# Kernel tuning notes

Hardware: AMD Instinct MI355X
Metric: run time of the kernel (lower is better)

## Reference

```python
import jax, jax.numpy as jnp
import numpy as np

N_NODES = 50000


def _gcn_layer(x, W, b, src, dst, n_nodes):
    # x: [N, Fin] -> h: [N, Fout]
    h = x @ W
    # symmetric normalization deg^{-1/2} A_hat deg^{-1/2} (self-loops already in src/dst)
    deg = jax.ops.segment_sum(jnp.ones(src.shape[0], h.dtype), dst, num_segments=n_nodes)
    dis = jnp.where(deg > 0, jax.lax.rsqrt(deg), jnp.zeros_like(deg))
    norm = dis[src] * dis[dst]  # [E]
    msg = h[src] * norm[:, None]  # [E, Fout]
    out = jax.ops.segment_sum(msg, dst, num_segments=n_nodes)
    return out + b


def setup_inputs() -> dict:
    key = jax.random.key(0)
    k1, k2, k3, k4 = jax.random.split(key, 4)
    in_ch, hid, out_ch = 128, 128, 64
    x = jax.random.normal(k1, (N_NODES, in_ch), dtype=jnp.float32)
    edge_index = jax.random.randint(k2, (2, 800000), 0, N_NODES, dtype=jnp.int64)
    # glorot-style init for the linear weights
    W1 = jax.random.normal(k3, (in_ch, hid), dtype=jnp.float32) * (1.0 / np.sqrt(in_ch))
    b1 = jnp.zeros((hid,), dtype=jnp.float32)
    W2 = jax.random.normal(k4, (hid, out_ch), dtype=jnp.float32) * (1.0 / np.sqrt(hid))
    b2 = jnp.zeros((out_ch,), dtype=jnp.float32)
    return {"x": x, "edge_index": edge_index, "W1": W1, "b1": b1, "W2": W2, "b2": b2}


def reference(x, edge_index, W1, b1, W2, b2):
    n = x.shape[0]
    loops = jnp.arange(n, dtype=edge_index.dtype)
    src = jnp.concatenate([edge_index[0], loops])
    dst = jnp.concatenate([edge_index[1], loops])
    h = jnp.tanh(_gcn_layer(x, W1, b1, src, dst, n))
    return _gcn_layer(h, W2, b2, src, dst, n)
```

## Files before the change

### kernel.cpp

```cpp
#include <hip/hip_runtime.h>
#include <math.h>


__global__ void detect_kernel(const int* __restrict__ ei32, int* __restrict__ flag) {
    if (blockIdx.x == 0 && threadIdx.x == 0) {
        int is64 = 1;
        for (int k = 1; k < 64; k += 2)
            if (ei32[k] != 0) { is64 = 0; break; }
        *flag = is64;
    }
}

__global__ __launch_bounds__(256) void normalize_kernel(const int* __restrict__ ei32,
                                                        const int* __restrict__ flag,
                                                        int* __restrict__ out, int n2,
                                                        int* __restrict__ hist, int nh) {
    const int is64 = *flag;
    for (int i = blockIdx.x * blockDim.x + threadIdx.x; i < n2;
         i += gridDim.x * blockDim.x) {
        out[i] = is64 ? ei32[2 * i] : ei32[i];
        if (i < nh) hist[i] = 0;
    }
}

__global__ __launch_bounds__(256) void hist_kernel(const int* __restrict__ dst, int E,
                                                   int* __restrict__ hist) {
    for (int i = blockIdx.x * blockDim.x + threadIdx.x; i < E;
         i += gridDim.x * blockDim.x) {
        atomicAdd(&hist[dst[i]], 1);
    }
}

__global__ __launch_bounds__(256) void scan1_kernel(const int* __restrict__ hist,
                                                    int* __restrict__ row_start,
                                                    int* __restrict__ partial, int n) {
    __shared__ int tmp[256];
    int t = threadIdx.x;
    int i = blockIdx.x * 256 + t;
    int v = (i < n) ? hist[i] : 0;
    tmp[t] = v;
    __syncthreads();
    for (int off = 1; off < 256; off <<= 1) {
        int add = (t >= off) ? tmp[t - off] : 0;
        __syncthreads();
        tmp[t] += add;
        __syncthreads();
    }
    if (i < n) row_start[i] = tmp[t] - v;
    if (t == 255) partial[blockIdx.x] = tmp[255];
}

__global__ __launch_bounds__(256) void scan2_kernel(const int* __restrict__ partial,
                                                    int* __restrict__ offsets, int nb) {
    __shared__ int tmp[256];
    int t = threadIdx.x;
    int v = (t < nb) ? partial[t] : 0;
    tmp[t] = v;
    __syncthreads();
    for (int off = 1; off < 256; off <<= 1) {
        int add = (t >= off) ? tmp[t - off] : 0;
        __syncthreads();
        tmp[t] += add;
        __syncthreads();
    }
    if (t < nb) offsets[t] = tmp[t] - v;
}

__global__ __launch_bounds__(256) void scan3_kernel(int* __restrict__ row_start,
                                                    const int* __restrict__ offsets,
                                                    const int* __restrict__ hist,
                                                    float* __restrict__ dis,
                                                    int* __restrict__ cursor,
                                                    int n, int E) {
    int i = blockIdx.x * 256 + threadIdx.x;
    if (i < n) {
        row_start[i] += offsets[i >> 8];
        dis[i] = rsqrtf((float)(hist[i] + 1));
        cursor[i] = 0;
    }
    if (i == 0) row_start[n] = E;
}

__global__ __launch_bounds__(256) void scatter_kernel(const int* __restrict__ src,
                                                      const int* __restrict__ dst, int E,
                                                      const int* __restrict__ row_start,
                                                      int* __restrict__ cursor,
                                                      int* __restrict__ csr_src) {
    for (int i = blockIdx.x * blockDim.x + threadIdx.x; i < E;
         i += gridDim.x * blockDim.x) {
        int d = dst[i];
        int pos = atomicAdd(&cursor[d], 1);
        csr_src[row_start[d] + pos] = src[i];
    }
}

template <int BM, int BN, int TM, int TN>
__global__ __launch_bounds__(256) void gemm_tile(const float* __restrict__ A,
                                                 const float* __restrict__ B,
                                                 const float* __restrict__ scale,
                                                 float* __restrict__ C,
                                                 int M, int K, int N) {
    constexpr int BK = 32;
    constexpr int TX = BN / TN;
    constexpr int TY = BM / TM;
    static_assert(TX * TY == 256, "256 threads");
    const int t = threadIdx.x;
    const int tx = t % TX;
    const int ty = t / TX;
    const int row0 = blockIdx.x * BM;

    __shared__ float As[BK][BM + 4];
    __shared__ float Bs[BK][BN + 4];

    float acc[TM][TN];
#pragma unroll
    for (int i = 0; i < TM; i++)
#pragma unroll
        for (int j = 0; j < TN; j++) acc[i][j] = 0.f;

    for (int k0 = 0; k0 < K; k0 += BK) {
        constexpr int A4 = BM * BK / 4;
#pragma unroll
        for (int idx4 = t; idx4 < A4; idx4 += 256) {
            int r = idx4 / (BK / 4);
            int c4 = idx4 % (BK / 4);
            float4 v = make_float4(0.f, 0.f, 0.f, 0.f);
            int gr = row0 + r;
            if (gr < M) v = *(const float4*)&A[(size_t)gr * K + k0 + c4 * 4];
            As[c4 * 4 + 0][r] = v.x;
            As[c4 * 4 + 1][r] = v.y;
            As[c4 * 4 + 2][r] = v.z;
            As[c4 * 4 + 3][r] = v.w;
        }
        constexpr int B4 = BK * BN / 4;
#pragma unroll
        for (int idx4 = t; idx4 < B4; idx4 += 256) {
            int r = idx4 / (BN / 4);
            int c4 = idx4 % (BN / 4);
            float4 v = *(const float4*)&B[(size_t)(k0 + r) * N + c4 * 4];
            *(float4*)&Bs[r][c4 * 4] = v;
        }
        __syncthreads();

#pragma unroll 4
        for (int kk = 0; kk < BK; kk++) {
            float a[TM], b[TN];
#pragma unroll
            for (int i = 0; i < TM; i += 4)
                *(float4*)&a[i] = *(const float4*)&As[kk][ty * TM + i];
#pragma unroll
            for (int j = 0; j < TN; j += 4)
                *(float4*)&b[j] = *(const float4*)&Bs[kk][tx * TN + j];
#pragma unroll
            for (int i = 0; i < TM; i++)
#pragma unroll
                for (int j = 0; j < TN; j++) acc[i][j] += a[i] * b[j];
        }
        __syncthreads();
    }

#pragma unroll
    for (int i = 0; i < TM; i++) {
        int gr = row0 + ty * TM + i;
        if (gr < M) {
            float sc = scale[gr];
#pragma unroll
            for (int j = 0; j < TN; j += 4) {
                float4 v = make_float4(acc[i][j] * sc, acc[i][j + 1] * sc,
                                       acc[i][j + 2] * sc, acc[i][j + 3] * sc);
                *(float4*)&C[(size_t)gr * N + tx * TN + j] = v;
            }
        }
    }
}

__global__ __launch_bounds__(256) void agg1_kernel(const float* __restrict__ hs,
                                                   const float* __restrict__ dis,
                                                   const int* __restrict__ row_start,
                                                   const int* __restrict__ csr_src,
                                                   const float* __restrict__ b1,
                                                   float* __restrict__ hout, int n) {
    int wid = threadIdx.x >> 6;
    int lane = threadIdx.x & 63;
    int node = blockIdx.x * 4 + wid;
    if (node >= n) return;

    const float2* hv = (const float2*)hs;
    float2 acc = hv[(size_t)node * 64 + lane];

    int e0 = row_start[node], e1 = row_start[node + 1];
    int e = e0;
    for (; e + 4 <= e1; e += 4) {
        int s0 = csr_src[e + 0];
        int s1 = csr_src[e + 1];
        int s2 = csr_src[e + 2];
        int s3 = csr_src[e + 3];
        float2 v0 = hv[(size_t)s0 * 64 + lane];
        float2 v1 = hv[(size_t)s1 * 64 + lane];
        float2 v2 = hv[(size_t)s2 * 64 + lane];
        float2 v3 = hv[(size_t)s3 * 64 + lane];
        acc.x += (v0.x + v1.x) + (v2.x + v3.x);
        acc.y += (v0.y + v1.y) + (v2.y + v3.y);
    }
    for (; e < e1; ++e) {
        int s = csr_src[e];
        float2 v = hv[(size_t)s * 64 + lane];
        acc.x += v.x;
        acc.y += v.y;
    }
    float dd = dis[node];
    float2 bb = ((const float2*)b1)[lane];
    float2 o;
    o.x = tanhf(acc.x * dd + bb.x);
    o.y = tanhf(acc.y * dd + bb.y);
    ((float2*)hout)[(size_t)node * 64 + lane] = o;
}

__global__ __launch_bounds__(256) void agg2_kernel(const float* __restrict__ hs,
                                                   const float* __restrict__ dis,
                                                   const int* __restrict__ row_start,
                                                   const int* __restrict__ csr_src,
                                                   const float* __restrict__ b2,
                                                   float* __restrict__ out, int n) {
    int wid = threadIdx.x >> 6;
    int lane = threadIdx.x & 63;
    int node = blockIdx.x * 4 + wid;
    if (node >= n) return;

    float acc = hs[(size_t)node * 64 + lane];

    int e0 = row_start[node], e1 = row_start[node + 1];
    int e = e0;
    for (; e + 4 <= e1; e += 4) {
        int s0 = csr_src[e + 0];
        int s1 = csr_src[e + 1];
        int s2 = csr_src[e + 2];
        int s3 = csr_src[e + 3];
        float v0 = hs[(size_t)s0 * 64 + lane];
        float v1 = hs[(size_t)s1 * 64 + lane];
        float v2 = hs[(size_t)s2 * 64 + lane];
        float v3 = hs[(size_t)s3 * 64 + lane];
        acc += (v0 + v1) + (v2 + v3);
    }
    for (; e < e1; ++e) {
        acc += hs[(size_t)csr_src[e] * 64 + lane];
    }
    out[(size_t)node * 64 + lane] = acc * dis[node] + b2[lane];
}

extern "C" void kernel_launch(void* const* d_in, const int* in_sizes, int n_in,
                              void* d_out, int out_size, void* d_ws, size_t ws_size,
                              hipStream_t stream) {
    const float* x  = (const float*)d_in[0];
    const int*   ei = (const int*)d_in[1];
    const float* W1 = (const float*)d_in[2];
    const float* b1 = (const float*)d_in[3];
    const float* W2 = (const float*)d_in[4];
    const float* b2 = (const float*)d_in[5];

    const int hid    = in_sizes[3];
    const int in_ch  = in_sizes[2] / hid;
    const int out_ch = in_sizes[5];
    const int N      = in_sizes[0] / in_ch;
    const int E      = in_sizes[1] / 2;

    char* wsp = (char*)d_ws;
    auto alloc = [&](size_t bytes) -> char* {
        char* p = wsp;
        wsp += (bytes + 255) & ~(size_t)255;
        return p;
    };
    float* h1        = (float*)alloc((size_t)N * hid * 4);
    float* hmid      = (float*)alloc((size_t)N * hid * 4);
    float* h2        = (float*)alloc((size_t)N * out_ch * 4);
    int*   hist      = (int*)alloc((size_t)N * 4);
    int*   cursor    = (int*)alloc((size_t)N * 4);
    int*   row_start = (int*)alloc((size_t)(N + 1) * 4);
    float* dis       = (float*)alloc((size_t)N * 4);
    int*   partial   = (int*)alloc(1024);
    int*   offsets   = (int*)alloc(1024);
    int*   flag      = (int*)alloc(256);
    int*   enorm     = (int*)alloc((size_t)2 * E * 4);
    int*   csr_src   = (int*)alloc((size_t)E * 4);

    const int NB = (N + 255) / 256;

    detect_kernel<<<1, 64, 0, stream>>>(ei, flag);
    normalize_kernel<<<2048, 256, 0, stream>>>(ei, flag, enorm, 2 * E, hist, N);
    const int* esrc = enorm;
    const int* edst = enorm + E;

    hist_kernel<<<1024, 256, 0, stream>>>(edst, E, hist);
    scan1_kernel<<<NB, 256, 0, stream>>>(hist, row_start, partial, N);
    scan2_kernel<<<1, 256, 0, stream>>>(partial, offsets, NB);
    scan3_kernel<<<NB, 256, 0, stream>>>(row_start, offsets, hist, dis, cursor, N, E);
    scatter_kernel<<<1024, 256, 0, stream>>>(esrc, edst, E, row_start, cursor, csr_src);

    gemm_tile<128, 128, 8, 8><<<(N + 127) / 128, 256, 0, stream>>>(x, W1, dis, h1, N, in_ch, hid);
    agg1_kernel<<<(N + 3) / 4, 256, 0, stream>>>(h1, dis, row_start, csr_src, b1, hmid, N);

    gemm_tile<128, 64, 8, 4><<<(N + 127) / 128, 256, 0, stream>>>(hmid, W2, dis, h2, N, hid, out_ch);
    agg2_kernel<<<(N + 3) / 4, 256, 0, stream>>>(h2, dis, row_start, csr_src, b2,
                                                 (float*)d_out, N);
}
```

Baseline: 321.3 us.

## Store GEMM outputs in fp16 to halve gather traffic in aggregation

The two GEMMs now write their scaled node features as fp16 instead of fp32, and both aggregation kernels gather fp16 rows and accumulate in fp32. This halves the bytes moved by the random-access neighbour gathers, which dominate the aggregation cost. Edge-format detection is folded into the normalize kernel, removing one launch, and the aggregation kernels switch to a fixed 1280-block grid-stride loop. The cost is reduced precision in the intermediate features, which may push results past the tolerance.

```diff
diff --git a/kernel.cpp b/kernel.cpp
--- a/kernel.cpp
+++ b/kernel.cpp
@@ -1,21 +1,20 @@
 #include <hip/hip_runtime.h>
+#include <hip/hip_fp16.h>
 #include <math.h>
 
 
-__global__ void detect_kernel(const int* __restrict__ ei32, int* __restrict__ flag) {
-    if (blockIdx.x == 0 && threadIdx.x == 0) {
+__global__ __launch_bounds__(256) void normalize_kernel(const int* __restrict__ ei32,
+                                                        int* __restrict__ out, int n2,
+                                                        int* __restrict__ hist, int nh) {
+    __shared__ int s_is64;
+    if (threadIdx.x == 0) {
         int is64 = 1;
         for (int k = 1; k < 64; k += 2)
             if (ei32[k] != 0) { is64 = 0; break; }
-        *flag = is64;
-    }
-}
-
-__global__ __launch_bounds__(256) void normalize_kernel(const int* __restrict__ ei32,
-                                                        const int* __restrict__ flag,
-                                                        int* __restrict__ out, int n2,
-                                                        int* __restrict__ hist, int nh) {
-    const int is64 = *flag;
+        s_is64 = is64;
+    }
+    __syncthreads();
+    const int is64 = s_is64;
     for (int i = blockIdx.x * blockDim.x + threadIdx.x; i < n2;
          i += gridDim.x * blockDim.x) {
         out[i] = is64 ? ei32[2 * i] : ei32[i];
@@ -94,11 +93,11 @@
     }
 }
 
-template <int BM, int BN, int TM, int TN>
+template <int BM, int BN, int TM, int TN, bool HALF_OUT>
 __global__ __launch_bounds__(256) void gemm_tile(const float* __restrict__ A,
                                                  const float* __restrict__ B,
                                                  const float* __restrict__ scale,
-                                                 float* __restrict__ C,
+                                                 void* __restrict__ Cv,
                                                  int M, int K, int N) {
     constexpr int BK = 32;
     constexpr int TX = BN / TN;
@@ -164,88 +163,101 @@
         int gr = row0 + ty * TM + i;
         if (gr < M) {
             float sc = scale[gr];
-#pragma unroll
-            for (int j = 0; j < TN; j += 4) {
-                float4 v = make_float4(acc[i][j] * sc, acc[i][j + 1] * sc,
-                                       acc[i][j + 2] * sc, acc[i][j + 3] * sc);
-                *(float4*)&C[(size_t)gr * N + tx * TN + j] = v;
+            if constexpr (HALF_OUT) {
+                __half* C = (__half*)Cv;
+                __half2 tmp[TN / 2];
+#pragma unroll
+                for (int j = 0; j < TN; j += 2)
+                    tmp[j / 2] = __floats2half2_rn(acc[i][j] * sc, acc[i][j + 1] * sc);
+                if constexpr (TN == 8) {
+                    *(float4*)&C[(size_t)gr * N + tx * TN] = *(float4*)tmp;
+                } else {
+                    *(float2*)&C[(size_t)gr * N + tx * TN] = *(float2*)tmp;
+                }
+            } else {
+                float* C = (float*)Cv;
+#pragma unroll
+                for (int j = 0; j < TN; j += 4) {
+                    float4 v = make_float4(acc[i][j] * sc, acc[i][j + 1] * sc,
+                                           acc[i][j + 2] * sc, acc[i][j + 3] * sc);
+                    *(float4*)&C[(size_t)gr * N + tx * TN + j] = v;
+                }
             }
         }
     }
 }
 
-__global__ __launch_bounds__(256) void agg1_kernel(const float* __restrict__ hs,
+__global__ __launch_bounds__(256) void agg1_kernel(const __half* __restrict__ hs,
                                                    const float* __restrict__ dis,
                                                    const int* __restrict__ row_start,
                                                    const int* __restrict__ csr_src,
                                                    const float* __restrict__ b1,
                                                    float* __restrict__ hout, int n) {
-    int wid = threadIdx.x >> 6;
-    int lane = threadIdx.x & 63;
-    int node = blockIdx.x * 4 + wid;
-    if (node >= n) return;
-
-    const float2* hv = (const float2*)hs;
-    float2 acc = hv[(size_t)node * 64 + lane];
-
-    int e0 = row_start[node], e1 = row_start[node + 1];
-    int e = e0;
-    for (; e + 4 <= e1; e += 4) {
-        int s0 = csr_src[e + 0];
-        int s1 = csr_src[e + 1];
-        int s2 = csr_src[e + 2];
-        int s3 = csr_src[e + 3];
-        float2 v0 = hv[(size_t)s0 * 64 + lane];
-        float2 v1 = hv[(size_t)s1 * 64 + lane];
-        float2 v2 = hv[(size_t)s2 * 64 + lane];
-        float2 v3 = hv[(size_t)s3 * 64 + lane];
-        acc.x += (v0.x + v1.x) + (v2.x + v3.x);
-        acc.y += (v0.y + v1.y) + (v2.y + v3.y);
-    }
-    for (; e < e1; ++e) {
-        int s = csr_src[e];
-        float2 v = hv[(size_t)s * 64 + lane];
-        acc.x += v.x;
-        acc.y += v.y;
-    }
-    float dd = dis[node];
-    float2 bb = ((const float2*)b1)[lane];
-    float2 o;
-    o.x = tanhf(acc.x * dd + bb.x);
-    o.y = tanhf(acc.y * dd + bb.y);
-    ((float2*)hout)[(size_t)node * 64 + lane] = o;
-}
-
-__global__ __launch_bounds__(256) void agg2_kernel(const float* __restrict__ hs,
+    const int wid = threadIdx.x >> 6;
+    const int lane = threadIdx.x & 63;
+    const __half2* hv = (const __half2*)hs;
+
+    for (int node = blockIdx.x * 4 + wid; node < n; node += gridDim.x * 4) {
+        float2 acc = __half22float2(hv[(size_t)node * 64 + lane]);
+
+        int e0 = row_start[node], e1 = row_start[node + 1];
+        int e = e0;
+        for (; e + 4 <= e1; e += 4) {
+            int s0 = csr_src[e + 0];
+            int s1 = csr_src[e + 1];
+            int s2 = csr_src[e + 2];
+            int s3 = csr_src[e + 3];
+            float2 v0 = __half22float2(hv[(size_t)s0 * 64 + lane]);
+            float2 v1 = __half22float2(hv[(size_t)s1 * 64 + lane]);
+            float2 v2 = __half22float2(hv[(size_t)s2 * 64 + lane]);
+            float2 v3 = __half22float2(hv[(size_t)s3 * 64 + lane]);
+            acc.x += (v0.x + v1.x) + (v2.x + v3.x);
+            acc.y += (v0.y + v1.y) + (v2.y + v3.y);
+        }
+        for (; e < e1; ++e) {
+            float2 v = __half22float2(hv[(size_t)csr_src[e] * 64 + lane]);
+            acc.x += v.x;
+            acc.y += v.y;
+        }
+        float dd = dis[node];
+        float2 bb = ((const float2*)b1)[lane];
+        float2 o;
+        o.x = tanhf(acc.x * dd + bb.x);
+        o.y = tanhf(acc.y * dd + bb.y);
+        ((float2*)hout)[(size_t)node * 64 + lane] = o;
+    }
+}
+
+__global__ __launch_bounds__(256) void agg2_kernel(const __half* __restrict__ hs,
                                                    const float* __restrict__ dis,
                                                    const int* __restrict__ row_start,
                                                    const int* __restrict__ csr_src,
                                                    const float* __restrict__ b2,
                                                    float* __restrict__ out, int n) {
-    int wid = threadIdx.x >> 6;
-    int lane = threadIdx.x & 63;
-    int node = blockIdx.x * 4 + wid;
-    if (node >= n) return;
-
-    float acc = hs[(size_t)node * 64 + lane];
-
-    int e0 = row_start[node], e1 = row_start[node + 1];
-    int e = e0;
-    for (; e + 4 <= e1; e += 4) {
-        int s0 = csr_src[e + 0];
-        int s1 = csr_src[e + 1];
-        int s2 = csr_src[e + 2];
-        int s3 = csr_src[e + 3];
-        float v0 = hs[(size_t)s0 * 64 + lane];
-        float v1 = hs[(size_t)s1 * 64 + lane];
-        float v2 = hs[(size_t)s2 * 64 + lane];
-        float v3 = hs[(size_t)s3 * 64 + lane];
-        acc += (v0 + v1) + (v2 + v3);
-    }
-    for (; e < e1; ++e) {
-        acc += hs[(size_t)csr_src[e] * 64 + lane];
-    }
-    out[(size_t)node * 64 + lane] = acc * dis[node] + b2[lane];
+    const int wid = threadIdx.x >> 6;
+    const int lane = threadIdx.x & 63;
+
+    for (int node = blockIdx.x * 4 + wid; node < n; node += gridDim.x * 4) {
+        float acc = __half2float(hs[(size_t)node * 64 + lane]);
+
+        int e0 = row_start[node], e1 = row_start[node + 1];
+        int e = e0;
+        for (; e + 4 <= e1; e += 4) {
+            int s0 = csr_src[e + 0];
+            int s1 = csr_src[e + 1];
+            int s2 = csr_src[e + 2];
+            int s3 = csr_src[e + 3];
+            float v0 = __half2float(hs[(size_t)s0 * 64 + lane]);
+            float v1 = __half2float(hs[(size_t)s1 * 64 + lane]);
+            float v2 = __half2float(hs[(size_t)s2 * 64 + lane]);
+            float v3 = __half2float(hs[(size_t)s3 * 64 + lane]);
+            acc += (v0 + v1) + (v2 + v3);
+        }
+        for (; e < e1; ++e) {
+            acc += __half2float(hs[(size_t)csr_src[e] * 64 + lane]);
+        }
+        out[(size_t)node * 64 + lane] = acc * dis[node] + b2[lane];
+    }
 }
 
 extern "C" void kernel_launch(void* const* d_in, const int* in_sizes, int n_in,
@@ -270,23 +282,21 @@
         wsp += (bytes + 255) & ~(size_t)255;
         return p;
     };
-    float* h1        = (float*)alloc((size_t)N * hid * 4);
-    float* hmid      = (float*)alloc((size_t)N * hid * 4);
-    float* h2        = (float*)alloc((size_t)N * out_ch * 4);
+    __half* h1       = (__half*)alloc((size_t)N * hid * 2);
+    float*  hmid     = (float*)alloc((size_t)N * hid * 4);
+    __half* h2       = (__half*)alloc((size_t)N * out_ch * 2);
     int*   hist      = (int*)alloc((size_t)N * 4);
     int*   cursor    = (int*)alloc((size_t)N * 4);
     int*   row_start = (int*)alloc((size_t)(N + 1) * 4);
     float* dis       = (float*)alloc((size_t)N * 4);
     int*   partial   = (int*)alloc(1024);
     int*   offsets   = (int*)alloc(1024);
-    int*   flag      = (int*)alloc(256);
     int*   enorm     = (int*)alloc((size_t)2 * E * 4);
     int*   csr_src   = (int*)alloc((size_t)E * 4);
 
     const int NB = (N + 255) / 256;
 
-    detect_kernel<<<1, 64, 0, stream>>>(ei, flag);
-    normalize_kernel<<<2048, 256, 0, stream>>>(ei, flag, enorm, 2 * E, hist, N);
+    normalize_kernel<<<2048, 256, 0, stream>>>(ei, enorm, 2 * E, hist, N);
     const int* esrc = enorm;
     const int* edst = enorm + E;
 
@@ -296,10 +306,12 @@
     scan3_kernel<<<NB, 256, 0, stream>>>(row_start, offsets, hist, dis, cursor, N, E);
     scatter_kernel<<<1024, 256, 0, stream>>>(esrc, edst, E, row_start, cursor, csr_src);
 
-    gemm_tile<128, 128, 8, 8><<<(N + 127) / 128, 256, 0, stream>>>(x, W1, dis, h1, N, in_ch, hid);
-    agg1_kernel<<<(N + 3) / 4, 256, 0, stream>>>(h1, dis, row_start, csr_src, b1, hmid, N);
-
-    gemm_tile<128, 64, 8, 4><<<(N + 127) / 128, 256, 0, stream>>>(hmid, W2, dis, h2, N, hid, out_ch);
-    agg2_kernel<<<(N + 3) / 4, 256, 0, stream>>>(h2, dis, row_start, csr_src, b2,
-                                                 (float*)d_out, N);
-}
+    gemm_tile<128, 128, 8, 8, true><<<(N + 127) / 128, 256, 0, stream>>>(
+        x, W1, dis, h1, N, in_ch, hid);
+    agg1_kernel<<<1280, 256, 0, stream>>>(h1, dis, row_start, csr_src, b1, hmid, N);
+
+    gemm_tile<128, 64, 8, 4, true><<<(N + 127) / 128, 256, 0, stream>>>(
+        hmid, W2, dis, h2, N, hid, out_ch);
+    agg2_kernel<<<1280, 256, 0, stream>>>(h2, dis, row_start, csr_src, b2,
+                                          (float*)d_out, N);
+}
```

Result: faster. 314.9 us (-2.0%).
